# Optimization experiments

Measured on AMD Instinct MI355X. Metric: run time of the kernel, lower is better.

The kernel has to match this reference:

```python
import jax, jax.numpy as jnp
import numpy as np

B, S, HID = 1, 2048, 2048
NH = 16
D_NOPE, D_ROPE, D_V = 128, 64, 128
D_QK = D_NOPE + D_ROPE            # 192
KV_R = 512                        # kv_lora_rank
EPS = 1e-6
SCALING = D_QK ** -0.5
NEG = -1e9


def rms_norm(x, w):
    xf = x.astype(jnp.float32)
    var = jnp.mean(xf * xf, axis=-1, keepdims=True)
    return w * (xf * jax.lax.rsqrt(var + EPS)).astype(x.dtype)


def rotate_half(x):
    x1, x2 = jnp.split(x, 2, axis=-1)
    return jnp.concatenate([-x2, x1], axis=-1)


def deinterleave(x):
    # torch: view(..., d//2, 2).transpose(-1, -2).reshape(..., d)
    # => [x0, x2, x4, ..., x1, x3, x5, ...]
    return jnp.concatenate([x[..., 0::2], x[..., 1::2]], axis=-1)


def setup_inputs() -> dict:
    key = jax.random.key(0)
    ks = jax.random.split(key, 6)
    hidden_states = jax.random.normal(ks[0], (B, S, HID), jnp.float32)
    # rotary cos/sin over qk_rope_head_dim
    inv_freq = 1.0 / (10000.0 ** (np.arange(0, D_ROPE, 2, dtype=np.float32) / D_ROPE))
    freqs = np.outer(np.arange(S, dtype=np.float32), inv_freq)   # [S, D_ROPE/2]
    emb = np.concatenate([freqs, freqs], axis=-1)                # [S, D_ROPE]
    cos = jnp.asarray(np.cos(emb), jnp.float32)[None]            # [1, S, D_ROPE]
    sin = jnp.asarray(np.sin(emb), jnp.float32)[None]
    # additive causal mask [1, 1, S, S]
    causal = np.where(np.tril(np.ones((S, S), dtype=bool)), 0.0, NEG).astype(np.float32)
    attention_mask = jnp.asarray(causal)[None, None]
    sc = lambda k, shp: jax.random.normal(k, shp, jnp.float32) * (shp[-1] ** -0.5)
    q_proj_w = sc(ks[1], (NH * D_QK, HID))
    kv_a_proj_w = sc(ks[2], (KV_R + D_ROPE, HID))
    kv_a_ln_w = jnp.ones((KV_R,), jnp.float32)
    kv_b_proj_w = sc(ks[3], (NH * (D_NOPE + D_V), KV_R))
    o_proj_w = sc(ks[4], (HID, NH * D_V))
    return dict(hidden_states=hidden_states, cos=cos, sin=sin,
                attention_mask=attention_mask, q_proj_w=q_proj_w,
                kv_a_proj_w=kv_a_proj_w, kv_a_ln_w=kv_a_ln_w,
                kv_b_proj_w=kv_b_proj_w, o_proj_w=o_proj_w)


def reference(hidden_states, cos, sin, attention_mask,
              q_proj_w, kv_a_proj_w, kv_a_ln_w, kv_b_proj_w, o_proj_w):
    b, s, _ = hidden_states.shape
    # Q projection -> [b, NH, s, D_QK]
    q = (hidden_states @ q_proj_w.T).reshape(b, s, NH, D_QK).transpose(0, 2, 1, 3)
    q_pass, q_rot = q[..., :D_NOPE], q[..., D_NOPE:]
    # compressed KV + shared rope key
    ckv = hidden_states @ kv_a_proj_w.T                           # [b, s, KV_R + D_ROPE]
    k_pass_c, k_rot = ckv[..., :KV_R], ckv[..., KV_R:]
    kv = (rms_norm(k_pass_c, kv_a_ln_w) @ kv_b_proj_w.T)
    kv = kv.reshape(b, s, NH, D_NOPE + D_V).transpose(0, 2, 1, 3)  # [b, NH, s, .]
    k_pass, value_states = kv[..., :D_NOPE], kv[..., D_NOPE:]
    k_rot = k_rot.reshape(b, 1, s, D_ROPE)
    # interleaved RoPE (rope_interleave=True)
    q_rot = deinterleave(q_rot)
    k_rot = deinterleave(k_rot)
    c = cos[:, None]  # [1, 1, s, D_ROPE]
    sn = sin[:, None]
    q_rot = q_rot * c + rotate_half(q_rot) * sn
    k_rot = k_rot * c + rotate_half(k_rot) * sn
    k_rot = jnp.broadcast_to(k_rot, (b, NH, s, D_ROPE))
    query_states = jnp.concatenate([q_pass, q_rot], axis=-1)      # [b, NH, s, D_QK]
    key_states = jnp.concatenate([k_pass, k_rot], axis=-1)
    # eager attention (num_key_value_groups == 1)
    scores = jnp.einsum('bhqd,bhkd->bhqk', query_states, key_states) * SCALING
    scores = scores + attention_mask[:, :, :, :s]
    attn = jax.nn.softmax(scores.astype(jnp.float32), axis=-1).astype(query_states.dtype)
    attn_out = jnp.einsum('bhqk,bhkd->bhqd', attn, value_states)  # [b, NH, s, D_V]
    attn_out = attn_out.transpose(0, 2, 1, 3).reshape(b, s, NH * D_V)
    return attn_out @ o_proj_w.T
```

## Files before the change

kernel.cpp:

```cpp
#include <hip/hip_runtime.h>
#include <hip/hip_bf16.h>
#include <stdint.h>
#include <stddef.h>

#define S_LEN 2048
#define HID_DIM 2048
#define NH 16
#define D_QK 192
#define D_NOPE 128
#define D_ROPE 64
#define D_V 128
#define KV_R 512
#define CKV_N (KV_R + D_ROPE)
#define KVB_N (NH * (D_NOPE + D_V))
#define QN (NH * D_QK)
#define CAT_N (QN + CKV_N)
#define SCALING 0.07216878364870322f

typedef __attribute__((ext_vector_type(8))) short short8;
typedef __attribute__((ext_vector_type(4))) short short4v;
typedef __attribute__((ext_vector_type(4))) float f32x4;

__device__ __forceinline__ short f2bf_bits(float f) {
  unsigned u = __float_as_uint(f);
  unsigned r = (u + 0x7fffu + ((u >> 16) & 1u)) >> 16;
  return (short)(r & 0xffffu);
}
__device__ __forceinline__ float bf2f(short b) {
  return __uint_as_float(((unsigned)(unsigned short)b) << 16);
}

__device__ __forceinline__ f32x4 mfma_bf16(short8 a, short8 b, f32x4 c) {
  return __builtin_amdgcn_mfma_f32_16x16x32_bf16(a, b, c, 0, 0, 0);
}

__global__ __launch_bounds__(256)
void cvt5_k(const float* __restrict__ s0, short* __restrict__ d0, int c0,
            const float* __restrict__ s1, short* __restrict__ d1, int c1,
            const float* __restrict__ s2, short* __restrict__ d2, int c2,
            const float* __restrict__ s3, short* __restrict__ d3, int c3,
            const float* __restrict__ s4, short* __restrict__ d4, int c4) {
  const int i = blockIdx.x * 256 + threadIdx.x;
  const float* s; short* d; int base;
  if      (i < c0) { s = s0; d = d0; base = 0;  }
  else if (i < c1) { s = s1; d = d1; base = c0; }
  else if (i < c2) { s = s2; d = d2; base = c1; }
  else if (i < c3) { s = s3; d = d3; base = c2; }
  else if (i < c4) { s = s4; d = d4; base = c3; }
  else return;
  const int j = i - base;
  const float4 v = ((const float4*)s)[j];
  short4v o;
  o.x = f2bf_bits(v.x); o.y = f2bf_bits(v.y);
  o.z = f2bf_bits(v.z); o.w = f2bf_bits(v.w);
  ((short4v*)d)[j] = o;
}

template <bool OUTF32>
__global__ __launch_bounds__(256, 3)
void gemm_bt(const short* __restrict__ A, const short* __restrict__ B,
             void* __restrict__ Cv, int M, int N, int K) {
  __shared__ short sA[2][128 * 32];
  __shared__ short sB[2][128 * 32];
  const int tid  = threadIdx.x;
  const int wave = tid >> 6;
  const int lane = tid & 63;
  const int bm = blockIdx.y * 128;
  const int bn = blockIdx.x * 128;
  const int wr = wave >> 1, wc = wave & 1;
  const int fr = lane & 15, fk = (lane >> 4) * 8;
  const int srow = lane >> 2;
  const int scol = (lane & 3) * 8;

  f32x4 acc[4][4];
  for (int i = 0; i < 4; ++i)
    for (int j = 0; j < 4; ++j)
      for (int r = 0; r < 4; ++r) acc[i][j][r] = 0.f;

  for (int k0 = 0; k0 < K; k0 += 64) {
    __syncthreads();
#pragma unroll
    for (int cc = 0; cc < 2; ++cc) {
      const int c = wave * 2 + cc;
      const int ar = bm + c * 16 + srow;
      int br = bn + c * 16 + srow; if (br > N - 1) br = N - 1;
#pragma unroll
      for (int kh = 0; kh < 2; ++kh) {
        __builtin_amdgcn_global_load_lds(
            (const __attribute__((address_space(1))) void*)(A + (size_t)ar * K + k0 + kh * 32 + scol),
            (__attribute__((address_space(3))) void*)(sA[kh] + c * 512), 16, 0, 0);
        __builtin_amdgcn_global_load_lds(
            (const __attribute__((address_space(1))) void*)(B + (size_t)br * K + k0 + kh * 32 + scol),
            (__attribute__((address_space(3))) void*)(sB[kh] + c * 512), 16, 0, 0);
      }
    }
    __syncthreads();
#pragma unroll
    for (int kh = 0; kh < 2; ++kh) {
      short8 af[4], bfr[4];
#pragma unroll
      for (int i = 0; i < 4; ++i)
        af[i] = *(const short8*)(sA[kh] + (wr * 64 + i * 16 + fr) * 32 + fk);
#pragma unroll
      for (int j = 0; j < 4; ++j)
        bfr[j] = *(const short8*)(sB[kh] + (wc * 64 + j * 16 + fr) * 32 + fk);
#pragma unroll
      for (int i = 0; i < 4; ++i)
#pragma unroll
        for (int j = 0; j < 4; ++j)
          acc[i][j] = mfma_bf16(af[i], bfr[j], acc[i][j]);
    }
  }

  const int cr = (lane >> 4) * 4, ccol = lane & 15;
#pragma unroll
  for (int i = 0; i < 4; ++i)
#pragma unroll
    for (int j = 0; j < 4; ++j) {
      const int col = bn + wc * 64 + j * 16 + ccol;
      if (col < N) {
#pragma unroll
        for (int r = 0; r < 4; ++r) {
          const int row = bm + wr * 64 + i * 16 + cr + r;
          if (OUTF32)
            ((float*)Cv)[(size_t)row * N + col] = acc[i][j][r];
          else
            ((short*)Cv)[(size_t)row * N + col] = f2bf_bits(acc[i][j][r]);
        }
      }
    }
}

__global__ __launch_bounds__(256)
void rmsnorm_k(const short* __restrict__ qckv, const float* __restrict__ w,
               short* __restrict__ out) {
  const int s = blockIdx.x, t = threadIdx.x;
  const short* x = qckv + (size_t)s * CAT_N + QN;
  float v0 = bf2f(x[2 * t]), v1 = bf2f(x[2 * t + 1]);
  float ss = v0 * v0 + v1 * v1;
#pragma unroll
  for (int off = 1; off < 64; off <<= 1) ss += __shfl_xor(ss, off, 64);
  __shared__ float red[4];
  if ((t & 63) == 0) red[t >> 6] = ss;
  __syncthreads();
  const float tot = red[0] + red[1] + red[2] + red[3];
  const float sc = rsqrtf(tot * (1.0f / 512.0f) + 1e-6f);
  out[(size_t)s * KV_R + 2 * t]     = f2bf_bits(v0 * sc * w[2 * t]);
  out[(size_t)s * KV_R + 2 * t + 1] = f2bf_bits(v1 * sc * w[2 * t + 1]);
}

__global__ __launch_bounds__(256)
void prep_k(const short* __restrict__ qckv, const short* __restrict__ kvb,
            const float* __restrict__ cosb, const float* __restrict__ sinb,
            short* __restrict__ Qs, short* __restrict__ Ks) {
  const int s = blockIdx.x, t = threadIdx.x;
  const short* qrow = qckv + (size_t)s * CAT_N;
  __shared__ float cs[32], sn[32];
  __shared__ short krs[64];
  if (t < 32) {
    const float c  = cosb[(size_t)s * 64 + t];
    const float si = sinb[(size_t)s * 64 + t];
    cs[t] = c; sn[t] = si;
    const float e0 = bf2f(qrow[QN + KV_R + 2 * t]);
    const float e1 = bf2f(qrow[QN + KV_R + 2 * t + 1]);
    krs[t]      = f2bf_bits(e0 * c - e1 * si);
    krs[t + 32] = f2bf_bits(e1 * c + e0 * si);
  }
  __syncthreads();
  const int h = t >> 4, i = t & 15;
  *(short8*)(Qs + ((size_t)h * S_LEN + s) * D_QK + i * 8) =
      *(const short8*)(qrow + h * D_QK + i * 8);
  *(short8*)(Ks + ((size_t)h * S_LEN + s) * D_QK + i * 8) =
      *(const short8*)(kvb + (size_t)s * KVB_N + h * 256 + i * 8);
#pragma unroll
  for (int p = 0; p < 2; ++p) {
    const int ii = i * 2 + p;
    const float e0 = bf2f(qrow[h * D_QK + 128 + 2 * ii]);
    const float e1 = bf2f(qrow[h * D_QK + 128 + 2 * ii + 1]);
    Qs[((size_t)h * S_LEN + s) * D_QK + 128 + ii] = f2bf_bits(e0 * cs[ii] - e1 * sn[ii]);
    Qs[((size_t)h * S_LEN + s) * D_QK + 160 + ii] = f2bf_bits(e1 * cs[ii] + e0 * sn[ii]);
  }
#pragma unroll
  for (int p = 0; p < 4; ++p) {
    const int idx = t * 4 + p;
    const int hh = idx >> 6, ii = idx & 63;
    Ks[((size_t)hh * S_LEN + s) * D_QK + 128 + ii] = krs[ii];
  }
}

__global__ __launch_bounds__(256)
void vtr_k(const short* __restrict__ kvb, short* __restrict__ Vt) {
  const int st = blockIdx.x, dt = blockIdx.y, h = blockIdx.z;
  __shared__ short sT[64][72];
  const int id = threadIdx.x;
#pragma unroll
  for (int p = 0; p < 2; ++p) {
    const int q = id + p * 256;
    const int row = q >> 3, c8 = q & 7;
    *(short8*)(&sT[row][c8 * 8]) =
        *(const short8*)(kvb + (size_t)(st * 64 + row) * KVB_N + h * 256 + 128 + dt * 64 + c8 * 8);
  }
  __syncthreads();
#pragma unroll
  for (int p = 0; p < 2; ++p) {
    const int q = id + p * 256;
    const int drow = q >> 3, c8 = q & 7;
    short8 o;
#pragma unroll
    for (int j = 0; j < 8; ++j) o[j] = sT[c8 * 8 + j][drow];
    *(short8*)(Vt + ((size_t)h * D_V + dt * 64 + drow) * S_LEN + st * 64 + c8 * 8) = o;
  }
}

__global__ __launch_bounds__(256, 2)
void flash_k(const short* __restrict__ Qs, const short* __restrict__ Ks,
             const short* __restrict__ Vt, short* __restrict__ Oc) {
  __shared__ short sK[64 * 200];
  __shared__ short sVt[128 * 72];
  __shared__ short P_lds[4][16 * 72];
  const int tid = threadIdx.x;
  const int wv = tid >> 6;
  const int lane = tid & 63;
  const int blk = blockIdx.x;
  const int h = ((blk & 7) << 1) | ((blk >> 3) & 1);
  const int qb = 31 - (blk >> 4);
  const int q0 = qb * 64 + wv * 16;
  const int fr = lane & 15, g = lane >> 4;

  const short* Qh = Qs + (size_t)h * S_LEN * D_QK;
  const short* Kh = Ks + (size_t)h * S_LEN * D_QK;
  const short* Vh = Vt + (size_t)h * D_V * S_LEN;

  int rowK[6], c8K[6], rowV[4], c8V[4];
#pragma unroll
  for (int p = 0; p < 6; ++p) {
    const int id = tid + p * 256;
    rowK[p] = id / 24; c8K[p] = id % 24;
  }
#pragma unroll
  for (int p = 0; p < 4; ++p) {
    const int id = tid + p * 256;
    rowV[p] = id >> 3; c8V[p] = id & 7;
  }

  short8 qa[6];
#pragma unroll
  for (int c = 0; c < 6; ++c)
    qa[c] = *(const short8*)(Qh + (size_t)(q0 + fr) * D_QK + c * 32 + g * 8);

  f32x4 o[8];
  for (int f = 0; f < 8; ++f)
    for (int r = 0; r < 4; ++r) o[f][r] = 0.f;
  float m_i[4] = {-1e30f, -1e30f, -1e30f, -1e30f};
  float l_i[4] = {0.f, 0.f, 0.f, 0.f};

  short8 kc[6], vc[4];
#pragma unroll
  for (int p = 0; p < 6; ++p)
    kc[p] = *(const short8*)(Kh + (size_t)rowK[p] * D_QK + c8K[p] * 8);
#pragma unroll
  for (int p = 0; p < 4; ++p)
    vc[p] = *(const short8*)(Vh + (size_t)rowV[p] * S_LEN + c8V[p] * 8);

  short* pl = &P_lds[wv][0];
  const int jn = qb + 1;
  for (int jt = 0; jt < jn; ++jt) {
    const int j0 = jt << 6;
    __syncthreads();
#pragma unroll
    for (int p = 0; p < 6; ++p)
      *(short8*)(sK + rowK[p] * 200 + c8K[p] * 8) = kc[p];
#pragma unroll
    for (int p = 0; p < 4; ++p)
      *(short8*)(sVt + rowV[p] * 72 + c8V[p] * 8) = vc[p];
    __syncthreads();
    if (jt + 1 < jn) {
      const int j1 = (jt + 1) << 6;
#pragma unroll
      for (int p = 0; p < 6; ++p)
        kc[p] = *(const short8*)(Kh + (size_t)(j1 + rowK[p]) * D_QK + c8K[p] * 8);
#pragma unroll
      for (int p = 0; p < 4; ++p)
        vc[p] = *(const short8*)(Vh + (size_t)rowV[p] * S_LEN + j1 + c8V[p] * 8);
    }

    f32x4 sc[4];
#pragma unroll
    for (int t = 0; t < 4; ++t)
      for (int r = 0; r < 4; ++r) sc[t][r] = -1e30f;
#pragma unroll
    for (int t = 0; t < 4; ++t) {
      if (j0 + t * 16 <= q0 + 15) {
        f32x4 a;
        for (int r = 0; r < 4; ++r) a[r] = 0.f;
        const short* kr = sK + (t * 16 + fr) * 200 + g * 8;
#pragma unroll
        for (int c = 0; c < 6; ++c)
          a = mfma_bf16(qa[c], *(const short8*)(kr + c * 32), a);
        sc[t] = a;
      }
    }
    float tm[4];
#pragma unroll
    for (int r = 0; r < 4; ++r) {
      const int row = q0 + g * 4 + r;
      float mx = -1e30f;
#pragma unroll
      for (int t = 0; t < 4; ++t) {
        const float v = (j0 + t * 16 + fr <= row) ? sc[t][r] * SCALING : -1e30f;
        sc[t][r] = v;
        mx = fmaxf(mx, v);
      }
      tm[r] = mx;
    }
#pragma unroll
    for (int off = 1; off < 16; off <<= 1)
#pragma unroll
      for (int r = 0; r < 4; ++r)
        tm[r] = fmaxf(tm[r], __shfl_xor(tm[r], off, 16));
    float ps[4];
#pragma unroll
    for (int r = 0; r < 4; ++r) {
      const float mnew = fmaxf(m_i[r], tm[r]);
      const float alpha = __expf(m_i[r] - mnew);
      m_i[r] = mnew;
      l_i[r] *= alpha;
      float s = 0.f;
#pragma unroll
      for (int t = 0; t < 4; ++t) {
        const float p = __expf(sc[t][r] - mnew);
        sc[t][r] = p;
        s += p;
      }
      ps[r] = s;
#pragma unroll
      for (int f = 0; f < 8; ++f) o[f][r] *= alpha;
    }
#pragma unroll
    for (int off = 1; off < 16; off <<= 1)
#pragma unroll
      for (int r = 0; r < 4; ++r)
        ps[r] += __shfl_xor(ps[r], off, 16);
#pragma unroll
    for (int r = 0; r < 4; ++r) l_i[r] += ps[r];

#pragma unroll
    for (int r = 0; r < 4; ++r)
#pragma unroll
      for (int t = 0; t < 4; ++t)
        pl[(g * 4 + r) * 72 + t * 16 + fr] = f2bf_bits(sc[t][r]);
    __builtin_amdgcn_fence(__ATOMIC_ACQ_REL, "wavefront");
    const short8 pa0 = *(const short8*)(pl + fr * 72 + g * 8);
    const short8 pa1 = *(const short8*)(pl + fr * 72 + 32 + g * 8);

#pragma unroll
    for (int f = 0; f < 8; ++f) {
      const short* vr = sVt + (f * 16 + fr) * 72 + g * 8;
      const short8 vb0 = *(const short8*)(vr);
      const short8 vb1 = *(const short8*)(vr + 32);
      o[f] = mfma_bf16(pa1, vb1, mfma_bf16(pa0, vb0, o[f]));
    }
  }

#pragma unroll
  for (int r = 0; r < 4; ++r) {
    const float inv = 1.0f / l_i[r];
    const int row = q0 + g * 4 + r;
#pragma unroll
    for (int f = 0; f < 8; ++f)
      Oc[(size_t)row * (NH * D_V) + h * D_V + f * 16 + fr] = f2bf_bits(o[f][r] * inv);
  }
}

extern "C" void kernel_launch(void* const* d_in, const int* in_sizes, int n_in,
                              void* d_out, int out_size, void* d_ws, size_t ws_size,
                              hipStream_t stream) {
  const float* hidden = (const float*)d_in[0];
  const float* cosb   = (const float*)d_in[1];
  const float* sinb   = (const float*)d_in[2];
  const float* q_w    = (const float*)d_in[4];
  const float* kva_w  = (const float*)d_in[5];
  const float* ln_w   = (const float*)d_in[6];
  const float* kvb_w  = (const float*)d_in[7];
  const float* o_w    = (const float*)d_in[8];
  float* out = (float*)d_out;

  char* ws = (char*)d_ws;
  size_t off = 0;
  auto alloc = [&](size_t elems) {
    short* p = (short*)(ws + off);
    off += ((elems * 2 + 255) & ~(size_t)255);
    return p;
  };
  short* hid_b   = alloc((size_t)S_LEN * HID_DIM);
  short* qkva_wb = alloc((size_t)CAT_N * HID_DIM);
  short* kvb_wb  = alloc((size_t)KVB_N * KV_R);
  short* o_wb    = alloc((size_t)HID_DIM * NH * D_V);
  short* qckv    = alloc((size_t)S_LEN * CAT_N);
  short* ckvn    = alloc((size_t)S_LEN * KV_R);
  short* kvb     = alloc((size_t)S_LEN * KVB_N);
  short* Qs      = alloc((size_t)NH * S_LEN * D_QK);
  short* Ks      = alloc((size_t)NH * S_LEN * D_QK);
  short* Vt      = alloc((size_t)NH * D_V * S_LEN);
  short* Oc      = alloc((size_t)S_LEN * NH * D_V);

  dim3 blk(256);
  const int n0 = (S_LEN * HID_DIM) / 4;
  const int n1 = (QN * HID_DIM) / 4;
  const int n2 = (CKV_N * HID_DIM) / 4;
  const int n3 = (KVB_N * KV_R) / 4;
  const int n4e = (HID_DIM * NH * D_V) / 4;
  const int c0 = n0, c1 = c0 + n1, c2 = c1 + n2, c3 = c2 + n3, c4 = c3 + n4e;
  cvt5_k<<<dim3((c4 + 255) / 256), blk, 0, stream>>>(
      hidden, hid_b, c0,
      q_w, qkva_wb, c1,
      kva_w, qkva_wb + (size_t)QN * HID_DIM, c2,
      kvb_w, kvb_wb, c3,
      o_w, o_wb, c4);

  gemm_bt<false><<<dim3((CAT_N + 127) / 128, S_LEN / 128), blk, 0, stream>>>(
      hid_b, qkva_wb, qckv, S_LEN, CAT_N, HID_DIM);
  rmsnorm_k<<<dim3(S_LEN), blk, 0, stream>>>(qckv, ln_w, ckvn);
  gemm_bt<false><<<dim3(KVB_N / 128, S_LEN / 128), blk, 0, stream>>>(
      ckvn, kvb_wb, kvb, S_LEN, KVB_N, KV_R);
  prep_k<<<dim3(S_LEN), blk, 0, stream>>>(qckv, kvb, cosb, sinb, Qs, Ks);
  vtr_k<<<dim3(S_LEN / 64, D_V / 64, NH), blk, 0, stream>>>(kvb, Vt);
  flash_k<<<dim3(NH * 128 / 4), blk, 0, stream>>>(Qs, Ks, Vt, Oc);
  gemm_bt<true><<<dim3(HID_DIM / 128, S_LEN / 128), blk, 0, stream>>>(
      Oc, o_wb, out, S_LEN, HID_DIM, NH * D_V);
}
```

Measured before the change: 312.9 us.

## Split long causal query blocks across KV halves and merge with combine kernel

Query blocks 16–31 of the causal flash kernel are now handled by two CTAs each: one covers KV tiles 0–15 and the other covers the remaining diagonal tiles. Each CTA writes unnormalized fp32 partial outputs plus its running max and sum to workspace, and a new combine kernel merges them with log-sum-exp weights and writes the bf16 output. This caps per-CTA work at 16 KV tiles, so long blocks no longer dominate the tail, and launch bounds are raised to allow 3 blocks per CU. The cost is an extra kernel launch and fp32 partial-result traffic. The partial buffers reuse the start of the workspace, which overlaps already-consumed bf16 buffers.

```diff
diff --git a/kernel.cpp b/kernel.cpp
--- a/kernel.cpp
+++ b/kernel.cpp
@@ -212,9 +212,10 @@
   }
 }
 
-__global__ __launch_bounds__(256, 2)
+__global__ __launch_bounds__(256, 3)
 void flash_k(const short* __restrict__ Qs, const short* __restrict__ Ks,
-             const short* __restrict__ Vt, short* __restrict__ Oc) {
+             const short* __restrict__ Vt, float* __restrict__ Op,
+             float* __restrict__ ml) {
   __shared__ short sK[64 * 200];
   __shared__ short sVt[128 * 72];
   __shared__ short P_lds[4][16 * 72];
@@ -223,7 +224,13 @@
   const int lane = tid & 63;
   const int blk = blockIdx.x;
   const int h = ((blk & 7) << 1) | ((blk >> 3) & 1);
-  const int qb = 31 - (blk >> 4);
+  const int c = blk >> 4;
+
+  int qb, jtBeg, jtEnd;
+  if (c < 16)      { qb = 16 + c; jtBeg = 0;  jtEnd = 16;     }
+  else if (c < 32) { qb = c;      jtBeg = 16; jtEnd = qb + 1; }
+  else             { qb = c - 32; jtBeg = 0;  jtEnd = qb + 1; }
+
   const int q0 = qb * 64 + wv * 16;
   const int fr = lane & 15, g = lane >> 4;
 
@@ -245,8 +252,8 @@
 
   short8 qa[6];
 #pragma unroll
-  for (int c = 0; c < 6; ++c)
-    qa[c] = *(const short8*)(Qh + (size_t)(q0 + fr) * D_QK + c * 32 + g * 8);
+  for (int cc = 0; cc < 6; ++cc)
+    qa[cc] = *(const short8*)(Qh + (size_t)(q0 + fr) * D_QK + cc * 32 + g * 8);
 
   f32x4 o[8];
   for (int f = 0; f < 8; ++f)
@@ -255,16 +262,18 @@
   float l_i[4] = {0.f, 0.f, 0.f, 0.f};
 
   short8 kc[6], vc[4];
-#pragma unroll
-  for (int p = 0; p < 6; ++p)
-    kc[p] = *(const short8*)(Kh + (size_t)rowK[p] * D_QK + c8K[p] * 8);
-#pragma unroll
-  for (int p = 0; p < 4; ++p)
-    vc[p] = *(const short8*)(Vh + (size_t)rowV[p] * S_LEN + c8V[p] * 8);
+  {
+    const int jb = jtBeg << 6;
+#pragma unroll
+    for (int p = 0; p < 6; ++p)
+      kc[p] = *(const short8*)(Kh + (size_t)(jb + rowK[p]) * D_QK + c8K[p] * 8);
+#pragma unroll
+    for (int p = 0; p < 4; ++p)
+      vc[p] = *(const short8*)(Vh + (size_t)rowV[p] * S_LEN + jb + c8V[p] * 8);
+  }
 
   short* pl = &P_lds[wv][0];
-  const int jn = qb + 1;
-  for (int jt = 0; jt < jn; ++jt) {
+  for (int jt = jtBeg; jt < jtEnd; ++jt) {
     const int j0 = jt << 6;
     __syncthreads();
 #pragma unroll
@@ -274,7 +283,7 @@
     for (int p = 0; p < 4; ++p)
       *(short8*)(sVt + rowV[p] * 72 + c8V[p] * 8) = vc[p];
     __syncthreads();
-    if (jt + 1 < jn) {
+    if (jt + 1 < jtEnd) {
       const int j1 = (jt + 1) << 6;
 #pragma unroll
       for (int p = 0; p < 6; ++p)
@@ -295,8 +304,8 @@
         for (int r = 0; r < 4; ++r) a[r] = 0.f;
         const short* kr = sK + (t * 16 + fr) * 200 + g * 8;
 #pragma unroll
-        for (int c = 0; c < 6; ++c)
-          a = mfma_bf16(qa[c], *(const short8*)(kr + c * 32), a);
+        for (int cc = 0; cc < 6; ++cc)
+          a = mfma_bf16(qa[cc], *(const short8*)(kr + cc * 32), a);
         sc[t] = a;
       }
     }
@@ -362,13 +371,57 @@
     }
   }
 
+  const int pid = h * 48 + c;
 #pragma unroll
   for (int r = 0; r < 4; ++r) {
-    const float inv = 1.0f / l_i[r];
-    const int row = q0 + g * 4 + r;
+    const int rr = wv * 16 + g * 4 + r;
 #pragma unroll
     for (int f = 0; f < 8; ++f)
-      Oc[(size_t)row * (NH * D_V) + h * D_V + f * 16 + fr] = f2bf_bits(o[f][r] * inv);
+      Op[((size_t)pid * 64 + rr) * 128 + f * 16 + fr] = o[f][r];
+    if (fr == 0) {
+      ml[((size_t)pid * 64 + rr) * 2 + 0] = m_i[r];
+      ml[((size_t)pid * 64 + rr) * 2 + 1] = l_i[r];
+    }
+  }
+}
+
+__global__ __launch_bounds__(256)
+void comb_k(const float* __restrict__ Op, const float* __restrict__ ml,
+            short* __restrict__ Oc) {
+  const int qb = blockIdx.x;
+  const int h  = blockIdx.y;
+  const int t  = threadIdx.x;
+  int pid0, pid1 = -1;
+  if (qb < 16) pid0 = h * 48 + 32 + qb;
+  else { pid0 = h * 48 + (qb - 16); pid1 = pid0 + 16; }
+#pragma unroll
+  for (int p = 0; p < 8; ++p) {
+    const int idx = t + p * 256;
+    const int row = idx >> 5;
+    const int c4  = idx & 31;
+    const float m0 = ml[(size_t)(pid0 * 64 + row) * 2 + 0];
+    const float l0 = ml[(size_t)(pid0 * 64 + row) * 2 + 1];
+    const float4 v0 = ((const float4*)(Op + ((size_t)pid0 * 64 + row) * 128))[c4];
+    float w0, w1 = 0.f;
+    float4 v1 = make_float4(0.f, 0.f, 0.f, 0.f);
+    if (pid1 >= 0) {
+      const float m1 = ml[(size_t)(pid1 * 64 + row) * 2 + 0];
+      const float l1 = ml[(size_t)(pid1 * 64 + row) * 2 + 1];
+      const float m  = fmaxf(m0, m1);
+      const float a0 = __expf(m0 - m), a1 = __expf(m1 - m);
+      const float inv = 1.0f / (l0 * a0 + l1 * a1);
+      w0 = a0 * inv; w1 = a1 * inv;
+      v1 = ((const float4*)(Op + ((size_t)pid1 * 64 + row) * 128))[c4];
+    } else {
+      w0 = 1.0f / l0;
+    }
+    const int grow = qb * 64 + row;
+    short4v o;
+    o.x = f2bf_bits(v0.x * w0 + v1.x * w1);
+    o.y = f2bf_bits(v0.y * w0 + v1.y * w1);
+    o.z = f2bf_bits(v0.z * w0 + v1.z * w1);
+    o.w = f2bf_bits(v0.w * w0 + v1.w * w1);
+    ((short4v*)(Oc + (size_t)grow * (NH * D_V) + h * D_V))[c4] = o;
   }
 }
 
@@ -404,6 +457,9 @@
   short* Vt      = alloc((size_t)NH * D_V * S_LEN);
   short* Oc      = alloc((size_t)S_LEN * NH * D_V);
 
+  float* Op_part = (float*)ws;
+  float* ml_part = (float*)(ws + (size_t)768 * 64 * 128 * 4);
+
   dim3 blk(256);
   const int n0 = (S_LEN * HID_DIM) / 4;
   const int n1 = (QN * HID_DIM) / 4;
@@ -425,7 +481,8 @@
       ckvn, kvb_wb, kvb, S_LEN, KVB_N, KV_R);
   prep_k<<<dim3(S_LEN), blk, 0, stream>>>(qckv, kvb, cosb, sinb, Qs, Ks);
   vtr_k<<<dim3(S_LEN / 64, D_V / 64, NH), blk, 0, stream>>>(kvb, Vt);
-  flash_k<<<dim3(NH * 128 / 4), blk, 0, stream>>>(Qs, Ks, Vt, Oc);
+  flash_k<<<dim3(NH * 48), blk, 0, stream>>>(Qs, Ks, Vt, Op_part, ml_part);
+  comb_k<<<dim3(32, 16), blk, 0, stream>>>(Op_part, ml_part, Oc);
   gemm_bt<true><<<dim3(HID_DIM / 128, S_LEN / 128), blk, 0, stream>>>(
       Oc, o_wb, out, S_LEN, HID_DIM, NH * D_V);
 }
```

New measurement: 331.5 us. 5.9% more time.

## Double-buffer GEMM LDS tiles to overlap global loads with MFMA

Applied to the files above, without the earlier changes.

Converts the bf16 GEMM main loop to a two-stage software pipeline. The next K-tile is issued via global_load_lds into a second LDS buffer while MFMAs run on the current one, with explicit vmcnt waits and barriers replacing the two syncthreads. The aim is to hide global memory latency behind compute. In exchange, LDS usage doubles and launch bounds drop from 3 to 2 blocks per SM, which reduces occupancy.

```diff
diff --git a/kernel.cpp b/kernel.cpp
--- a/kernel.cpp
+++ b/kernel.cpp
@@ -57,11 +57,11 @@
 }
 
 template <bool OUTF32>
-__global__ __launch_bounds__(256, 3)
+__global__ __launch_bounds__(256, 2)
 void gemm_bt(const short* __restrict__ A, const short* __restrict__ B,
              void* __restrict__ Cv, int M, int N, int K) {
-  __shared__ short sA[2][128 * 32];
-  __shared__ short sB[2][128 * 32];
+  __shared__ short sA[2][2][128 * 32];
+  __shared__ short sB[2][2][128 * 32];
   const int tid  = threadIdx.x;
   const int wave = tid >> 6;
   const int lane = tid & 63;
@@ -72,44 +72,59 @@
   const int srow = lane >> 2;
   const int scol = (lane & 3) * 8;
 
+  auto stage = [&](int buf, int kt) {
+    const int k0 = kt << 6;
+#pragma unroll
+    for (int cc = 0; cc < 2; ++cc) {
+      const int c = wave * 2 + cc;
+      const int ar = bm + c * 16 + srow;
+      int br = bn + c * 16 + srow; if (br > N - 1) br = N - 1;
+#pragma unroll
+      for (int kh = 0; kh < 2; ++kh) {
+        __builtin_amdgcn_global_load_lds(
+            (const __attribute__((address_space(1))) void*)(A + (size_t)ar * K + k0 + kh * 32 + scol),
+            (__attribute__((address_space(3))) void*)(&sA[buf][kh][c * 512]), 16, 0, 0);
+        __builtin_amdgcn_global_load_lds(
+            (const __attribute__((address_space(1))) void*)(B + (size_t)br * K + k0 + kh * 32 + scol),
+            (__attribute__((address_space(3))) void*)(&sB[buf][kh][c * 512]), 16, 0, 0);
+      }
+    }
+  };
+
   f32x4 acc[4][4];
   for (int i = 0; i < 4; ++i)
     for (int j = 0; j < 4; ++j)
       for (int r = 0; r < 4; ++r) acc[i][j][r] = 0.f;
 
-  for (int k0 = 0; k0 < K; k0 += 64) {
-    __syncthreads();
-#pragma unroll
-    for (int cc = 0; cc < 2; ++cc) {
-      const int c = wave * 2 + cc;
-      const int ar = bm + c * 16 + srow;
-      int br = bn + c * 16 + srow; if (br > N - 1) br = N - 1;
-#pragma unroll
-      for (int kh = 0; kh < 2; ++kh) {
-        __builtin_amdgcn_global_load_lds(
-            (const __attribute__((address_space(1))) void*)(A + (size_t)ar * K + k0 + kh * 32 + scol),
-            (__attribute__((address_space(3))) void*)(sA[kh] + c * 512), 16, 0, 0);
-        __builtin_amdgcn_global_load_lds(
-            (const __attribute__((address_space(1))) void*)(B + (size_t)br * K + k0 + kh * 32 + scol),
-            (__attribute__((address_space(3))) void*)(sB[kh] + c * 512), 16, 0, 0);
-      }
-    }
-    __syncthreads();
+  const int nk = K >> 6;
+  stage(0, 0);
+  for (int kt = 0; kt < nk; ++kt) {
+    const int cur = kt & 1;
+    if (kt + 1 < nk) {
+      stage(cur ^ 1, kt + 1);
+      asm volatile("s_waitcnt vmcnt(8)" ::: "memory");
+    } else {
+      asm volatile("s_waitcnt vmcnt(0)" ::: "memory");
+    }
+    __builtin_amdgcn_s_barrier();
+    asm volatile("" ::: "memory");
 #pragma unroll
     for (int kh = 0; kh < 2; ++kh) {
       short8 af[4], bfr[4];
 #pragma unroll
       for (int i = 0; i < 4; ++i)
-        af[i] = *(const short8*)(sA[kh] + (wr * 64 + i * 16 + fr) * 32 + fk);
+        af[i] = *(const short8*)(&sA[cur][kh][(wr * 64 + i * 16 + fr) * 32 + fk]);
 #pragma unroll
       for (int j = 0; j < 4; ++j)
-        bfr[j] = *(const short8*)(sB[kh] + (wc * 64 + j * 16 + fr) * 32 + fk);
+        bfr[j] = *(const short8*)(&sB[cur][kh][(wc * 64 + j * 16 + fr) * 32 + fk]);
 #pragma unroll
       for (int i = 0; i < 4; ++i)
 #pragma unroll
         for (int j = 0; j < 4; ++j)
           acc[i][j] = mfma_bf16(af[i], bfr[j], acc[i][j]);
     }
+    asm volatile("" ::: "memory");
+    __builtin_amdgcn_s_barrier();
   }
 
   const int cr = (lane >> 4) * 4, ccol = lane & 15;
```

Result: no change. 315.7 us (+0.9%).

## Replace GEMM with 256x256 8-wave pipelined kernel using swizzled LDS

Applied to the files above, without the earlier changes.

Replaces the 128x128 four-wave GEMM with a 256x256 tile, 512-thread kernel. It uses XOR-swizzled LDS, double-buffered global-to-LDS prefetch interleaved across eight compute phases, explicit vmcnt waits, and s_setprio around MFMA bursts. The fused Q/KV-A weight is zero-padded to 3840 rows so N divides the tile, and the qckv leading dimension changes to match. The aim is to hide load latency and cut LDS bank conflicts, at the cost of padded extra work, a per-call memset, and fewer blocks for the smaller GEMMs.

```diff
diff --git a/kernel.cpp b/kernel.cpp
--- a/kernel.cpp
+++ b/kernel.cpp
@@ -15,6 +15,8 @@
 #define KVB_N (NH * (D_NOPE + D_V))
 #define QN (NH * D_QK)
 #define CAT_N (QN + CKV_N)
+#define QKVA_ROWS 3840
+#define QCKV_LD QKVA_ROWS
 #define SCALING 0.07216878364870322f
 
 typedef __attribute__((ext_vector_type(8))) short short8;
@@ -33,6 +35,12 @@
 __device__ __forceinline__ f32x4 mfma_bf16(short8 a, short8 b, f32x4 c) {
   return __builtin_amdgcn_mfma_f32_16x16x32_bf16(a, b, c, 0, 0, 0);
 }
+
+#define BARRIER_FENCED() do { \
+    asm volatile("" ::: "memory"); \
+    __builtin_amdgcn_s_barrier(); \
+    asm volatile("" ::: "memory"); \
+  } while (0)
 
 __global__ __launch_bounds__(256)
 void cvt5_k(const float* __restrict__ s0, short* __restrict__ d0, int c0,
@@ -57,85 +65,145 @@
 }
 
 template <bool OUTF32>
-__global__ __launch_bounds__(256, 3)
-void gemm_bt(const short* __restrict__ A, const short* __restrict__ B,
+__global__ __launch_bounds__(512, 2)
+void gemm8_k(const short* __restrict__ A, const short* __restrict__ B,
              void* __restrict__ Cv, int M, int N, int K) {
-  __shared__ short sA[2][128 * 32];
-  __shared__ short sB[2][128 * 32];
+  __shared__ short lds[2][2][2][128 * 64];
   const int tid  = threadIdx.x;
-  const int wave = tid >> 6;
+  const int wid  = tid >> 6;
   const int lane = tid & 63;
-  const int bm = blockIdx.y * 128;
-  const int bn = blockIdx.x * 128;
-  const int wr = wave >> 1, wc = wave & 1;
-  const int fr = lane & 15, fk = (lane >> 4) * 8;
-  const int srow = lane >> 2;
-  const int scol = (lane & 3) * 8;
-
-  f32x4 acc[4][4];
-  for (int i = 0; i < 4; ++i)
-    for (int j = 0; j < 4; ++j)
-      for (int r = 0; r < 4; ++r) acc[i][j][r] = 0.f;
-
-  for (int k0 = 0; k0 < K; k0 += 64) {
-    __syncthreads();
-#pragma unroll
-    for (int cc = 0; cc < 2; ++cc) {
-      const int c = wave * 2 + cc;
-      const int ar = bm + c * 16 + srow;
-      int br = bn + c * 16 + srow; if (br > N - 1) br = N - 1;
-#pragma unroll
-      for (int kh = 0; kh < 2; ++kh) {
-        __builtin_amdgcn_global_load_lds(
-            (const __attribute__((address_space(1))) void*)(A + (size_t)ar * K + k0 + kh * 32 + scol),
-            (__attribute__((address_space(3))) void*)(sA[kh] + c * 512), 16, 0, 0);
-        __builtin_amdgcn_global_load_lds(
-            (const __attribute__((address_space(1))) void*)(B + (size_t)br * K + k0 + kh * 32 + scol),
-            (__attribute__((address_space(3))) void*)(sB[kh] + c * 512), 16, 0, 0);
+  const int wa = wid >> 2;
+  const int wb = wid & 3;
+  const int fr = lane & 15;
+  const int g  = lane >> 4;
+  const int bm = blockIdx.y * 256;
+  const int bn = blockIdx.x * 256;
+  const int nk = K >> 6;
+
+  auto stage_half = [&](int buf, int ab, int half, int kt) {
+    const short* P = ab ? B : A;
+    const int rowbase = (ab ? bn : bm) + half * 128;
+    const int k0 = kt << 6;
+#pragma unroll
+    for (int p = 0; p < 2; ++p) {
+      const int c = p * 512 + tid;
+      const int r = c >> 3;
+      const int sc = ((c & 7) ^ (r & 7)) << 3;
+      __builtin_amdgcn_global_load_lds(
+          (const __attribute__((address_space(1))) void*)(P + (size_t)(rowbase + r) * K + k0 + sc),
+          (__attribute__((address_space(3))) void*)(&lds[buf][ab][half][(p * 512 + (wid << 6)) * 8]),
+          16, 0, 0);
+    }
+  };
+
+  f32x4 acc[2][2][4][2];
+#pragma unroll
+  for (int mh = 0; mh < 2; ++mh)
+#pragma unroll
+    for (int nh = 0; nh < 2; ++nh)
+#pragma unroll
+      for (int mi = 0; mi < 4; ++mi)
+#pragma unroll
+        for (int nj = 0; nj < 2; ++nj)
+          for (int r = 0; r < 4; ++r) acc[mh][nh][mi][nj][r] = 0.f;
+
+  stage_half(0, 0, 0, 0); stage_half(0, 0, 1, 0);
+  stage_half(0, 1, 0, 0); stage_half(0, 1, 1, 0);
+  stage_half(1, 0, 0, 1); stage_half(1, 1, 0, 1);
+  asm volatile("s_waitcnt vmcnt(4)" ::: "memory");
+  BARRIER_FENCED();
+
+  for (int it = 0; it < (nk >> 1); ++it) {
+    const int T = it << 1;
+#pragma unroll
+    for (int tt = 0; tt < 2; ++tt) {
+#pragma unroll
+      for (int q = 0; q < 4; ++q) {
+        const int ph = tt * 4 + q;
+        const int mh = q >> 1, nh = q & 1;
+
+        short8 af[4][2], bfm[2][2];
+#pragma unroll
+        for (int mi = 0; mi < 4; ++mi) {
+          const int lr = wa * 64 + mi * 16 + fr;
+#pragma unroll
+          for (int kh = 0; kh < 2; ++kh) {
+            const int byte = lr * 128 + kh * 64 + g * 16;
+            const int phys = byte ^ ((lr & 7) << 4);
+            af[mi][kh] = *(const short8*)((const char*)&lds[tt][0][mh][0] + phys);
+          }
+        }
+#pragma unroll
+        for (int nj = 0; nj < 2; ++nj) {
+          const int lc = wb * 32 + nj * 16 + fr;
+#pragma unroll
+          for (int kh = 0; kh < 2; ++kh) {
+            const int byte = lc * 128 + kh * 64 + g * 16;
+            const int phys = byte ^ ((lc & 7) << 4);
+            bfm[nj][kh] = *(const short8*)((const char*)&lds[tt][1][nh][0] + phys);
+          }
+        }
+
+        if (ph == 0) stage_half(1, 0, 1, T + 1);
+        if (ph == 1) stage_half(1, 1, 1, T + 1);
+        if (ph == 2 && T + 2 < nk) stage_half(0, 0, 0, T + 2);
+        if (ph == 3 && T + 2 < nk) stage_half(0, 1, 0, T + 2);
+        if (ph == 4 && T + 2 < nk) stage_half(0, 0, 1, T + 2);
+        if (ph == 5 && T + 2 < nk) stage_half(0, 1, 1, T + 2);
+        if (ph == 6 && T + 3 < nk) stage_half(1, 0, 0, T + 3);
+        if (ph == 7 && T + 3 < nk) stage_half(1, 1, 0, T + 3);
+
+        BARRIER_FENCED();
+
+        __builtin_amdgcn_s_setprio(1);
+#pragma unroll
+        for (int mi = 0; mi < 4; ++mi)
+#pragma unroll
+          for (int nj = 0; nj < 2; ++nj)
+#pragma unroll
+            for (int kh = 0; kh < 2; ++kh)
+              acc[mh][nh][mi][nj] = mfma_bf16(af[mi][kh], bfm[nj][kh], acc[mh][nh][mi][nj]);
+        __builtin_amdgcn_s_setprio(0);
+
+        if (ph == 3) {
+          if (T + 2 < nk) asm volatile("s_waitcnt vmcnt(4)" ::: "memory");
+          else            asm volatile("s_waitcnt vmcnt(0)" ::: "memory");
+        }
+        if (ph == 7) {
+          if (T + 3 < nk) asm volatile("s_waitcnt vmcnt(4)" ::: "memory");
+          else            asm volatile("s_waitcnt vmcnt(0)" ::: "memory");
+        }
+        BARRIER_FENCED();
       }
     }
-    __syncthreads();
-#pragma unroll
-    for (int kh = 0; kh < 2; ++kh) {
-      short8 af[4], bfr[4];
-#pragma unroll
-      for (int i = 0; i < 4; ++i)
-        af[i] = *(const short8*)(sA[kh] + (wr * 64 + i * 16 + fr) * 32 + fk);
-#pragma unroll
-      for (int j = 0; j < 4; ++j)
-        bfr[j] = *(const short8*)(sB[kh] + (wc * 64 + j * 16 + fr) * 32 + fk);
-#pragma unroll
-      for (int i = 0; i < 4; ++i)
-#pragma unroll
-        for (int j = 0; j < 4; ++j)
-          acc[i][j] = mfma_bf16(af[i], bfr[j], acc[i][j]);
-    }
   }
 
   const int cr = (lane >> 4) * 4, ccol = lane & 15;
 #pragma unroll
-  for (int i = 0; i < 4; ++i)
-#pragma unroll
-    for (int j = 0; j < 4; ++j) {
-      const int col = bn + wc * 64 + j * 16 + ccol;
-      if (col < N) {
-#pragma unroll
-        for (int r = 0; r < 4; ++r) {
-          const int row = bm + wr * 64 + i * 16 + cr + r;
-          if (OUTF32)
-            ((float*)Cv)[(size_t)row * N + col] = acc[i][j][r];
-          else
-            ((short*)Cv)[(size_t)row * N + col] = f2bf_bits(acc[i][j][r]);
+  for (int mh = 0; mh < 2; ++mh)
+#pragma unroll
+    for (int nh = 0; nh < 2; ++nh)
+#pragma unroll
+      for (int mi = 0; mi < 4; ++mi)
+#pragma unroll
+        for (int nj = 0; nj < 2; ++nj) {
+          const int row0 = bm + mh * 128 + wa * 64 + mi * 16 + cr;
+          const int col  = bn + nh * 128 + wb * 32 + nj * 16 + ccol;
+#pragma unroll
+          for (int r = 0; r < 4; ++r) {
+            if (OUTF32)
+              ((float*)Cv)[(size_t)(row0 + r) * N + col] = acc[mh][nh][mi][nj][r];
+            else
+              ((short*)Cv)[(size_t)(row0 + r) * N + col] = f2bf_bits(acc[mh][nh][mi][nj][r]);
+          }
         }
-      }
-    }
 }
 
 __global__ __launch_bounds__(256)
 void rmsnorm_k(const short* __restrict__ qckv, const float* __restrict__ w,
                short* __restrict__ out) {
   const int s = blockIdx.x, t = threadIdx.x;
-  const short* x = qckv + (size_t)s * CAT_N + QN;
+  const short* x = qckv + (size_t)s * QCKV_LD + QN;
   float v0 = bf2f(x[2 * t]), v1 = bf2f(x[2 * t + 1]);
   float ss = v0 * v0 + v1 * v1;
 #pragma unroll
@@ -154,7 +222,7 @@
             const float* __restrict__ cosb, const float* __restrict__ sinb,
             short* __restrict__ Qs, short* __restrict__ Ks) {
   const int s = blockIdx.x, t = threadIdx.x;
-  const short* qrow = qckv + (size_t)s * CAT_N;
+  const short* qrow = qckv + (size_t)s * QCKV_LD;
   __shared__ float cs[32], sn[32];
   __shared__ short krs[64];
   if (t < 32) {
@@ -393,10 +461,10 @@
     return p;
   };
   short* hid_b   = alloc((size_t)S_LEN * HID_DIM);
-  short* qkva_wb = alloc((size_t)CAT_N * HID_DIM);
+  short* qkva_wb = alloc((size_t)QKVA_ROWS * HID_DIM);
   short* kvb_wb  = alloc((size_t)KVB_N * KV_R);
   short* o_wb    = alloc((size_t)HID_DIM * NH * D_V);
-  short* qckv    = alloc((size_t)S_LEN * CAT_N);
+  short* qckv    = alloc((size_t)S_LEN * QCKV_LD);
   short* ckvn    = alloc((size_t)S_LEN * KV_R);
   short* kvb     = alloc((size_t)S_LEN * KVB_N);
   short* Qs      = alloc((size_t)NH * S_LEN * D_QK);
@@ -405,6 +473,9 @@
   short* Oc      = alloc((size_t)S_LEN * NH * D_V);
 
   dim3 blk(256);
+  hipMemsetAsync(qkva_wb + (size_t)CAT_N * HID_DIM, 0,
+                 (size_t)(QKVA_ROWS - CAT_N) * HID_DIM * 2, stream);
+
   const int n0 = (S_LEN * HID_DIM) / 4;
   const int n1 = (QN * HID_DIM) / 4;
   const int n2 = (CKV_N * HID_DIM) / 4;
@@ -418,14 +489,14 @@
       kvb_w, kvb_wb, c3,
       o_w, o_wb, c4);
 
-  gemm_bt<false><<<dim3((CAT_N + 127) / 128, S_LEN / 128), blk, 0, stream>>>(
-      hid_b, qkva_wb, qckv, S_LEN, CAT_N, HID_DIM);
+  gemm8_k<false><<<dim3(QKVA_ROWS / 256, S_LEN / 256), dim3(512), 0, stream>>>(
+      hid_b, qkva_wb, qckv, S_LEN, QKVA_ROWS, HID_DIM);
   rmsnorm_k<<<dim3(S_LEN), blk, 0, stream>>>(qckv, ln_w, ckvn);
-  gemm_bt<false><<<dim3(KVB_N / 128, S_LEN / 128), blk, 0, stream>>>(
+  gemm8_k<false><<<dim3(KVB_N / 256, S_LEN / 256), dim3(512), 0, stream>>>(
       ckvn, kvb_wb, kvb, S_LEN, KVB_N, KV_R);
   prep_k<<<dim3(S_LEN), blk, 0, stream>>>(qckv, kvb, cosb, sinb, Qs, Ks);
   vtr_k<<<dim3(S_LEN / 64, D_V / 64, NH), blk, 0, stream>>>(kvb, Vt);
   flash_k<<<dim3(NH * 128 / 4), blk, 0, stream>>>(Qs, Ks, Vt, Oc);
-  gemm_bt<true><<<dim3(HID_DIM / 128, S_LEN / 128), blk, 0, stream>>>(
+  gemm8_k<true><<<dim3(HID_DIM / 256, S_LEN / 256), dim3(512), 0, stream>>>(
       Oc, o_wb, out, S_LEN, HID_DIM, NH * D_V);
 }
```

Result: slower. 374.4 us (+19.6%).
